# Kernel tuning notes

Measured on AMD Instinct MI355X. Metric: run time of the kernel, lower is better.

The kernel has to match this reference:

```python
import jax, jax.numpy as jnp
import numpy as np

HIDDEN = 896
N_HEADS = 14
N_KV = 2
HEAD_DIM = HIDDEN // N_HEADS  # 64
N_REP = N_HEADS // N_KV       # 7
ROPE_THETA = 1000000.0


def setup_inputs() -> dict:
    key = jax.random.key(0)
    ks = jax.random.split(key, 8)
    B, S = 2, 2048
    s = 0.02
    return {
        "hidden_states": jax.random.normal(ks[0], (B, S, HIDDEN), dtype=jnp.float32),
        "position_ids": jnp.broadcast_to(jnp.arange(S, dtype=jnp.int64), (B, S)),
        "Wq": jax.random.normal(ks[1], (HIDDEN, HIDDEN), dtype=jnp.float32) * s,
        "bq": jnp.zeros((HIDDEN,), dtype=jnp.float32),
        "Wk": jax.random.normal(ks[2], (N_KV * HEAD_DIM, HIDDEN), dtype=jnp.float32) * s,
        "bk": jnp.zeros((N_KV * HEAD_DIM,), dtype=jnp.float32),
        "Wv": jax.random.normal(ks[3], (N_KV * HEAD_DIM, HIDDEN), dtype=jnp.float32) * s,
        "bv": jnp.zeros((N_KV * HEAD_DIM,), dtype=jnp.float32),
        "Wo": jax.random.normal(ks[4], (HIDDEN, HIDDEN), dtype=jnp.float32) * s,
    }


def _rotate_half(x):
    x1, x2 = x[..., : HEAD_DIM // 2], x[..., HEAD_DIM // 2 :]
    return jnp.concatenate((-x2, x1), axis=-1)


def reference(hidden_states, position_ids, Wq, bq, Wk, bk, Wv, bv, Wo):
    B, S, _ = hidden_states.shape
    q = (hidden_states @ Wq.T + bq).reshape(B, S, N_HEADS, HEAD_DIM)
    k = (hidden_states @ Wk.T + bk).reshape(B, S, N_KV, HEAD_DIM)
    v = (hidden_states @ Wv.T + bv).reshape(B, S, N_KV, HEAD_DIM)

    # RoPE: cos/sin [B, S, 1, HEAD_DIM]
    inv_freq = 1.0 / (ROPE_THETA ** (jnp.arange(0, HEAD_DIM, 2, dtype=jnp.float32) / HEAD_DIM))
    freqs = position_ids.astype(jnp.float32)[..., None] * inv_freq  # [B,S,D/2]
    emb = jnp.concatenate((freqs, freqs), axis=-1)
    cos = jnp.cos(emb)[:, :, None, :]
    sin = jnp.sin(emb)[:, :, None, :]
    q = q * cos + _rotate_half(q) * sin
    k = k * cos + _rotate_half(k) * sin

    # [B, H, S, D]; repeat KV heads (GQA)
    q = q.transpose(0, 2, 1, 3)
    k = jnp.repeat(k.transpose(0, 2, 1, 3), N_REP, axis=1)
    v = jnp.repeat(v.transpose(0, 2, 1, 3), N_REP, axis=1)

    scale = 1.0 / np.sqrt(HEAD_DIM)
    scores = jnp.einsum("bhqd,bhkd->bhqk", q, k) * scale
    causal = jnp.tril(jnp.ones((S, S), dtype=bool))
    scores = jnp.where(causal[None, None, :, :], scores, jnp.finfo(scores.dtype).min)
    probs = jax.nn.softmax(scores, axis=-1)
    attn = jnp.einsum("bhqk,bhkd->bhqd", probs, v)  # [B,H,S,D]
    attn = attn.transpose(0, 2, 1, 3).reshape(B, S, HIDDEN)
    return attn @ Wo.T
```

## Files before the change

kernel.cpp:

```cpp
#include <hip/hip_runtime.h>

#define HID 896
#define NH 14
#define NKV 2
#define NREP 7
#define SEQ 2048
#define BT 2
#define NTOK (BT*SEQ)
#define CSCALE 0.18033688011112042f

typedef __attribute__((ext_vector_type(8))) short bf16x8;
typedef __attribute__((ext_vector_type(8))) unsigned short u16x8;
typedef __attribute__((ext_vector_type(4))) float fx4;
typedef __attribute__((ext_vector_type(4))) short s16x4;
typedef _Float16 f16x4 __attribute__((ext_vector_type(4)));
typedef __fp16 fp16x2 __attribute__((ext_vector_type(2)));

__device__ __forceinline__ unsigned short f2b(float x){
  union { float f; unsigned u; } a; a.f = x;
  unsigned r = a.u + 0x7FFFu + ((a.u >> 16) & 1u);
  return (unsigned short)(r >> 16);
}
__device__ __forceinline__ unsigned short f2h(float x){
  union { _Float16 h; unsigned short u; } a; a.h = (_Float16)x; return a.u;
}

__global__ __launch_bounds__(256) void cvt_kernel(
    const float* __restrict__ s0, const float* __restrict__ s1,
    const float* __restrict__ s2, const float* __restrict__ s3,
    const float* __restrict__ s4,
    unsigned short* __restrict__ d0, unsigned short* __restrict__ d1,
    unsigned short* __restrict__ d2, unsigned short* __restrict__ d3,
    unsigned short* __restrict__ d4,
    int c0, int c1, int c2, int c3, int c4)
{
  const float* s; unsigned short* d; int c;
  switch (blockIdx.y){
    case 0: s=s0; d=d0; c=c0; break;
    case 1: s=s1; d=d1; c=c1; break;
    case 2: s=s2; d=d2; c=c2; break;
    case 3: s=s3; d=d3; c=c3; break;
    default: s=s4; d=d4; c=c4; break;
  }
  for (int i = (blockIdx.x*256 + threadIdx.x)*8; i < c; i += gridDim.x*2048){
    float4 a = *(const float4*)(s + i);
    float4 b = *(const float4*)(s + i + 4);
    u16x8 o;
    o[0]=f2b(a.x); o[1]=f2b(a.y); o[2]=f2b(a.z); o[3]=f2b(a.w);
    o[4]=f2b(b.x); o[5]=f2b(b.y); o[6]=f2b(b.z); o[7]=f2b(b.w);
    *(u16x8*)(d + i) = o;
  }
}

__global__ __launch_bounds__(256) void qkv_gemm_kernel(
    const unsigned short* __restrict__ A, const unsigned short* __restrict__ Bw,
    const float* __restrict__ bq, const float* __restrict__ bk, const float* __restrict__ bv,
    const int* __restrict__ pos,
    unsigned short* __restrict__ qo, unsigned short* __restrict__ ko,
    unsigned short* __restrict__ vt)
{
  __shared__ short As[64*72];
  __shared__ short Bs[128*72];
  const int tid = threadIdx.x;
  const int bm = blockIdx.x, bn = blockIdx.y;
  const int w = tid >> 6, l = tid & 63, l15 = l & 15, q4 = l >> 4;
  const int wm = w >> 1, wn = w & 1;

  fx4 acc[2][4] = {};

  const int srow = tid >> 3, scol = (tid & 7)*8;
  const unsigned short* Ag = A  + (size_t)(bm*64  + srow)*HID + scol;
  const unsigned short* Bg = Bw + (size_t)(bn*128 + srow)*HID + scol;

  u16x8 ar[2], br[4];
#pragma unroll
  for (int p = 0; p < 2; p++) ar[p] = *(const u16x8*)(Ag + (size_t)p*32*HID);
#pragma unroll
  for (int p = 0; p < 4; p++) br[p] = *(const u16x8*)(Bg + (size_t)p*32*HID);

  for (int kt = 0; kt < 14; kt++){
#pragma unroll
    for (int p = 0; p < 2; p++) *(u16x8*)&As[(srow + p*32)*72 + scol] = ar[p];
#pragma unroll
    for (int p = 0; p < 4; p++) *(u16x8*)&Bs[(srow + p*32)*72 + scol] = br[p];
    __syncthreads();
    if (kt < 13){
      const int ko_ = (kt+1)*64;
#pragma unroll
      for (int p = 0; p < 2; p++) ar[p] = *(const u16x8*)(Ag + (size_t)p*32*HID + ko_);
#pragma unroll
      for (int p = 0; p < 4; p++) br[p] = *(const u16x8*)(Bg + (size_t)p*32*HID + ko_);
    }
#pragma unroll
    for (int ks = 0; ks < 2; ks++){
      bf16x8 af[2], bf[4];
#pragma unroll
      for (int mt = 0; mt < 2; mt++)
        af[mt] = *(bf16x8*)&As[(wm*32 + mt*16 + l15)*72 + ks*32 + q4*8];
#pragma unroll
      for (int nt = 0; nt < 4; nt++)
        bf[nt] = *(bf16x8*)&Bs[(wn*64 + nt*16 + l15)*72 + ks*32 + q4*8];
#pragma unroll
      for (int mt = 0; mt < 2; mt++)
#pragma unroll
        for (int nt = 0; nt < 4; nt++)
          acc[mt][nt] = __builtin_amdgcn_mfma_f32_16x16x32_bf16(af[mt], bf[nt], acc[mt][nt], 0,0,0);
    }
    __syncthreads();
  }

  const int hu = bn*2 + wn;
  const float* bias; int kind, hloc;
  if (hu < NH)      { bias = bq + hu*64;      kind = 0; hloc = hu; }
  else if (hu < 16) { bias = bk + (hu-NH)*64; kind = 1; hloc = hu-NH; }
  else              { bias = bv + (hu-16)*64; kind = 2; hloc = hu-16; }
  float bl[4];
#pragma unroll
  for (int nt = 0; nt < 4; nt++) bl[nt] = bias[nt*16 + l15];

  if (kind == 2){
#pragma unroll
    for (int mt = 0; mt < 2; mt++)
#pragma unroll
      for (int j = 0; j < 4; j++){
        int grow = bm*64 + wm*32 + mt*16 + q4*4 + j;
        int b = grow >> 11, s = grow & (SEQ-1);
        int tile = s >> 6, key = s & 63;
        unsigned short* dst = vt + (size_t)(((b*NKV + hloc)*(SEQ/64) + tile)*4096);
#pragma unroll
        for (int nt = 0; nt < 4; nt++)
          dst[(nt*16 + l15)*64 + key] = f2h(acc[mt][nt][j] + bl[nt]);
      }
  } else {
    float invf[2];
#pragma unroll
    for (int nt = 0; nt < 2; nt++)
      invf[nt] = exp2f(-(float)(nt*16 + l15) * 0.62286151779138041f);
#pragma unroll
    for (int mt = 0; mt < 2; mt++)
#pragma unroll
      for (int j = 0; j < 4; j++){
        int grow = bm*64 + wm*32 + mt*16 + q4*4 + j;
        int b = grow >> 11, s = grow & (SEQ-1);
        float p = (float)pos[grow];
        unsigned short* dst = (kind == 0)
            ? qo + ((size_t)(b*NH  + hloc)*SEQ + s)*64
            : ko + ((size_t)(b*NKV + hloc)*SEQ + s)*64;
#pragma unroll
        for (int nt = 0; nt < 2; nt++){
          int d = nt*16 + l15;
          float f = p * invf[nt];
          float sv, cv;
          sincosf(f, &sv, &cv);
          float x1 = acc[mt][nt][j]   + bl[nt];
          float x2 = acc[mt][nt+2][j] + bl[nt+2];
          dst[d]    = f2b(x1*cv - x2*sv);
          dst[d+32] = f2b(x2*cv + x1*sv);
        }
      }
  }
}

__device__ __forceinline__ void smax_pv(
    const fx4* s, bool diag, int wl, int q4,
    float& m_run, float& l_run, fx4* o, const f16x4 vf[4][4])
{
  float tv[16];
#pragma unroll
  for (int tl = 0; tl < 4; tl++)
#pragma unroll
    for (int j = 0; j < 4; j++){
      float x = s[tl][j]*CSCALE;
      if (diag && (tl*16 + q4*4 + j > wl)) x = -1e30f;
      tv[tl*4+j] = x;
    }
  float mx = tv[0];
#pragma unroll
  for (int i = 1; i < 16; i++) mx = fmaxf(mx, tv[i]);
  mx = fmaxf(mx, __shfl_xor(mx, 16));
  mx = fmaxf(mx, __shfl_xor(mx, 32));
  float mn = fmaxf(m_run, mx);
  float al = exp2f(m_run - mn);
  m_run = mn;
  float p[16], rs = 0.f;
#pragma unroll
  for (int i = 0; i < 16; i++){ p[i] = exp2f(tv[i] - mn); rs += p[i]; }
  rs += __shfl_xor(rs, 16);
  rs += __shfl_xor(rs, 32);
  l_run = l_run*al + rs;
#pragma unroll
  for (int nt = 0; nt < 4; nt++)
#pragma unroll
    for (int j = 0; j < 4; j++) o[nt][j] *= al;
  f16x4 pf[4];
#pragma unroll
  for (int tl = 0; tl < 4; tl++){
    union { f16x4 v; fp16x2 h[2]; } u;
    u.h[0] = __builtin_amdgcn_cvt_pkrtz(p[tl*4+0], p[tl*4+1]);
    u.h[1] = __builtin_amdgcn_cvt_pkrtz(p[tl*4+2], p[tl*4+3]);
    pf[tl] = u.v;
  }
#pragma unroll
  for (int nt = 0; nt < 4; nt++)
#pragma unroll
    for (int tl = 0; tl < 4; tl++)
      o[nt] = __builtin_amdgcn_mfma_f32_16x16x16f16(vf[nt][tl], pf[tl], o[nt], 0,0,0);
}

__global__ __launch_bounds__(512) void attn_kernel(
    const unsigned short* __restrict__ q, const unsigned short* __restrict__ k,
    const unsigned short* __restrict__ vt, unsigned short* __restrict__ ao)
{
  __shared__ short SB[4*64*72];
  short* KsB = SB;
  short* VtB = SB + 2*64*72;

  const int tid = threadIdx.x;
  const int w = tid >> 6, l = tid & 63, l15 = l & 15, q4 = l >> 4;
  const int g = w >> 2, wi = w & 3;
  const int tlo = blockIdx.x, thi = 31 - tlo;
  const int h = blockIdx.y, b = blockIdx.z, kvh = h / NREP;
  const int wl = wi*16 + l15;

  const unsigned short* qbase = q + ((size_t)(b*NH + h)*SEQ)*64;
  const unsigned short* qpA = qbase + (size_t)(thi*64 + wl)*64;
  const unsigned short* qpB = qbase + (size_t)(tlo*64 + wl)*64;
  bf16x8 qA0 = *(const bf16x8*)(qpA + q4*8), qA1 = *(const bf16x8*)(qpA + 32 + q4*8);
  bf16x8 qB0 = *(const bf16x8*)(qpB + q4*8), qB1 = *(const bf16x8*)(qpB + 32 + q4*8);

  fx4 oA[4] = {}, oB[4] = {};
  float mA = -1e30f, lA = 0.f, mB = -1e30f, lB = 0.f;

  const unsigned short* kbase = k  + ((size_t)(b*NKV + kvh)*SEQ)*64;
  const unsigned short* vbase = vt + (size_t)((b*NKV + kvh)*(SEQ/64))*4096;

  const int P = (thi + 2) >> 1;

  u16x8 kreg[2], vreg[2];
#pragma unroll
  for (int p = 0; p < 2; p++){
    int idx = p*512 + tid, tile = idx >> 9, off = idx & 511;
    kreg[p] = *(const u16x8*)(kbase + (size_t)tile*4096 + off*8);
    vreg[p] = *(const u16x8*)(vbase + (size_t)tile*4096 + off*8);
  }

  for (int si = 0; si < P; si++){
#pragma unroll
    for (int p = 0; p < 2; p++){
      int idx = p*512 + tid, tile = idx >> 9, off = idx & 511;
      int rr = off >> 3, g8 = off & 7;
      *(u16x8*)&KsB[tile*4608 + rr*72 + g8*8] = kreg[p];
      *(u16x8*)&VtB[tile*4608 + rr*72 + g8*8] = vreg[p];
    }
    __syncthreads();

    if (si + 1 < P){
      const int k0n = 2*(si+1);
#pragma unroll
      for (int p = 0; p < 2; p++){
        int idx = p*512 + tid, tile = idx >> 9, off = idx & 511;
        int tk = k0n + tile; if (tk > thi) tk = thi;
        kreg[p] = *(const u16x8*)(kbase + (size_t)tk*4096 + off*8);
        vreg[p] = *(const u16x8*)(vbase + (size_t)tk*4096 + off*8);
      }
    }

    const int kt = 2*si + g;
    if (kt <= thi){
      const short* Kst = KsB + g*4608;
      const short* Vtt = VtB + g*4608;
      bf16x8 kf0[4], kf1[4];
#pragma unroll
      for (int tl = 0; tl < 4; tl++){
        kf0[tl] = *(const bf16x8*)&Kst[(tl*16 + l15)*72 + q4*8];
        kf1[tl] = *(const bf16x8*)&Kst[(tl*16 + l15)*72 + 32 + q4*8];
      }
      f16x4 vf[4][4];
#pragma unroll
      for (int nt = 0; nt < 4; nt++)
#pragma unroll
        for (int tl = 0; tl < 4; tl++)
          vf[nt][tl] = *(const f16x4*)&Vtt[(nt*16 + l15)*72 + tl*16 + q4*4];

      {
        fx4 s[4] = {};
#pragma unroll
        for (int tl = 0; tl < 4; tl++){
          s[tl] = __builtin_amdgcn_mfma_f32_16x16x32_bf16(kf0[tl], qA0, s[tl], 0,0,0);
          s[tl] = __builtin_amdgcn_mfma_f32_16x16x32_bf16(kf1[tl], qA1, s[tl], 0,0,0);
        }
        smax_pv(s, kt == thi, wl, q4, mA, lA, oA, vf);
      }
      if (kt <= tlo){
        fx4 s[4] = {};
#pragma unroll
        for (int tl = 0; tl < 4; tl++){
          s[tl] = __builtin_amdgcn_mfma_f32_16x16x32_bf16(kf0[tl], qB0, s[tl], 0,0,0);
          s[tl] = __builtin_amdgcn_mfma_f32_16x16x32_bf16(kf1[tl], qB1, s[tl], 0,0,0);
        }
        smax_pv(s, kt == tlo, wl, q4, mB, lB, oB, vf);
      }
    }
    __syncthreads();
  }

  float* F = (float*)SB;
  if (g == 1){
    float* fa = F + (((wi*2 + 0)*64 + l)*18);
#pragma unroll
    for (int nt = 0; nt < 4; nt++)
#pragma unroll
      for (int j = 0; j < 4; j++) fa[nt*4 + j] = oA[nt][j];
    fa[16] = mA; fa[17] = lA;
    float* fb = F + (((wi*2 + 1)*64 + l)*18);
#pragma unroll
    for (int nt = 0; nt < 4; nt++)
#pragma unroll
      for (int j = 0; j < 4; j++) fb[nt*4 + j] = oB[nt][j];
    fb[16] = mB; fb[17] = lB;
  }
  __syncthreads();
  if (g == 0){
    {
      const float* fa = F + (((wi*2 + 0)*64 + l)*18);
      float m1 = fa[16], l1 = fa[17];
      float mM = fmaxf(mA, m1);
      float a0 = exp2f(mA - mM), a1 = exp2f(m1 - mM);
      lA = lA*a0 + l1*a1;
#pragma unroll
      for (int nt = 0; nt < 4; nt++)
#pragma unroll
        for (int j = 0; j < 4; j++) oA[nt][j] = oA[nt][j]*a0 + fa[nt*4+j]*a1;
    }
    {
      const float* fb = F + (((wi*2 + 1)*64 + l)*18);
      float m1 = fb[16], l1 = fb[17];
      float mM = fmaxf(mB, m1);
      float a0 = exp2f(mB - mM), a1 = exp2f(m1 - mM);
      lB = lB*a0 + l1*a1;
#pragma unroll
      for (int nt = 0; nt < 4; nt++)
#pragma unroll
        for (int j = 0; j < 4; j++) oB[nt][j] = oB[nt][j]*a0 + fb[nt*4+j]*a1;
    }
    {
      float inv = 1.0f / lA;
      unsigned short* dst = ao + ((size_t)(b*SEQ + thi*64 + wl))*HID + h*64;
#pragma unroll
      for (int nt = 0; nt < 4; nt++){
        s16x4 ov;
        ov[0] = (short)f2b(oA[nt][0]*inv); ov[1] = (short)f2b(oA[nt][1]*inv);
        ov[2] = (short)f2b(oA[nt][2]*inv); ov[3] = (short)f2b(oA[nt][3]*inv);
        *(s16x4*)(dst + nt*16 + q4*4) = ov;
      }
    }
    {
      float inv = 1.0f / lB;
      unsigned short* dst = ao + ((size_t)(b*SEQ + tlo*64 + wl))*HID + h*64;
#pragma unroll
      for (int nt = 0; nt < 4; nt++){
        s16x4 ov;
        ov[0] = (short)f2b(oB[nt][0]*inv); ov[1] = (short)f2b(oB[nt][1]*inv);
        ov[2] = (short)f2b(oB[nt][2]*inv); ov[3] = (short)f2b(oB[nt][3]*inv);
        *(s16x4*)(dst + nt*16 + q4*4) = ov;
      }
    }
  }
}

__global__ __launch_bounds__(256) void out_gemm_kernel(
    const unsigned short* __restrict__ A, const unsigned short* __restrict__ Bw,
    float* __restrict__ out)
{
  __shared__ short As[64*72];
  __shared__ short Bs[128*72];
  const int tid = threadIdx.x;
  const int bm = blockIdx.x, bn = blockIdx.y;
  const int w = tid >> 6, l = tid & 63, l15 = l & 15, q4 = l >> 4;
  const int wm = w >> 1, wn = w & 1;

  fx4 acc[2][4] = {};

  const int srow = tid >> 3, scol = (tid & 7)*8;
  const unsigned short* Ag = A  + (size_t)(bm*64  + srow)*HID + scol;
  const unsigned short* Bg = Bw + (size_t)(bn*128 + srow)*HID + scol;

  u16x8 ar[2], br[4];
#pragma unroll
  for (int p = 0; p < 2; p++) ar[p] = *(const u16x8*)(Ag + (size_t)p*32*HID);
#pragma unroll
  for (int p = 0; p < 4; p++) br[p] = *(const u16x8*)(Bg + (size_t)p*32*HID);

  for (int kt = 0; kt < 14; kt++){
#pragma unroll
    for (int p = 0; p < 2; p++) *(u16x8*)&As[(srow + p*32)*72 + scol] = ar[p];
#pragma unroll
    for (int p = 0; p < 4; p++) *(u16x8*)&Bs[(srow + p*32)*72 + scol] = br[p];
    __syncthreads();
    if (kt < 13){
      const int ko_ = (kt+1)*64;
#pragma unroll
      for (int p = 0; p < 2; p++) ar[p] = *(const u16x8*)(Ag + (size_t)p*32*HID + ko_);
#pragma unroll
      for (int p = 0; p < 4; p++) br[p] = *(const u16x8*)(Bg + (size_t)p*32*HID + ko_);
    }
#pragma unroll
    for (int ks = 0; ks < 2; ks++){
      bf16x8 af[2], bf[4];
#pragma unroll
      for (int mt = 0; mt < 2; mt++)
        af[mt] = *(bf16x8*)&As[(wm*32 + mt*16 + l15)*72 + ks*32 + q4*8];
#pragma unroll
      for (int nt = 0; nt < 4; nt++)
        bf[nt] = *(bf16x8*)&Bs[(wn*64 + nt*16 + l15)*72 + ks*32 + q4*8];
#pragma unroll
      for (int mt = 0; mt < 2; mt++)
#pragma unroll
        for (int nt = 0; nt < 4; nt++)
          acc[mt][nt] = __builtin_amdgcn_mfma_f32_16x16x32_bf16(af[mt], bf[nt], acc[mt][nt], 0,0,0);
    }
    __syncthreads();
  }

#pragma unroll
  for (int mt = 0; mt < 2; mt++)
#pragma unroll
    for (int j = 0; j < 4; j++){
      int grow = bm*64 + wm*32 + mt*16 + q4*4 + j;
      float* dst = out + (size_t)grow*HID + bn*128 + wn*64;
#pragma unroll
      for (int nt = 0; nt < 4; nt++)
        dst[nt*16 + l15] = acc[mt][nt][j];
    }
}

extern "C" void kernel_launch(void* const* d_in, const int* in_sizes, int n_in,
                              void* d_out, int out_size, void* d_ws, size_t ws_size,
                              hipStream_t stream)
{
  const float* hidden = (const float*)d_in[0];
  const int*   pos    = (const int*)d_in[1];
  const float* Wq = (const float*)d_in[2]; const float* bq = (const float*)d_in[3];
  const float* Wk = (const float*)d_in[4]; const float* bk = (const float*)d_in[5];
  const float* Wv = (const float*)d_in[6]; const float* bv = (const float*)d_in[7];
  const float* Wo = (const float*)d_in[8];

  unsigned short* qws   = (unsigned short*)d_ws;
  unsigned short* kws   = qws   + (size_t)BT*NH*SEQ*64;
  unsigned short* vtws  = kws   + (size_t)BT*NKV*SEQ*64;
  unsigned short* wqkv  = vtws  + (size_t)BT*NKV*SEQ*64;
  unsigned short* wo16  = wqkv  + (size_t)1152*HID;
  unsigned short* h16   = wo16  + (size_t)HID*HID;

  const int nh   = NTOK*HID;
  const int nwq  = HID*HID;
  const int nwkv = 2*64*HID;

  cvt_kernel<<<dim3(448, 5), 256, 0, stream>>>(
      hidden, Wq, Wk, Wv, Wo,
      h16, wqkv, wqkv + nwq, wqkv + nwq + nwkv, wo16,
      nh, nwq, nwkv, nwkv, nwq);

  qkv_gemm_kernel<<<dim3(NTOK/64, 9), 256, 0, stream>>>(
      h16, wqkv, bq, bk, bv, pos, qws, kws, vtws);

  attn_kernel<<<dim3(16, NH, BT), 512, 0, stream>>>(qws, kws, vtws, h16 );

  out_gemm_kernel<<<dim3(NTOK/64, 7), 256, 0, stream>>>(h16 , wo16, (float*)d_out);
}
```

Baseline: 171.7 us.

## Fuse hidden-state bf16 conversion into QKV GEMM, precompute RoPE table, fold scale

Removes the separate fp32-to-bf16 conversion pass over hidden states by loading fp32 directly in the QKV GEMM and converting while staging into shared memory. A cos/sin RoPE table is built in the weight-conversion kernel so the GEMM epilogue does lookups instead of sincosf. The softmax scale is folded into Q in the epilogue, and both GEMMs move to a 128-wide K tile with 7 iterations instead of 14. The cost is more registers for the larger staging buffers, larger LDS tiles, and a table indexed by position that assumes positions are below SEQ.

```diff
diff --git a/kernel.cpp b/kernel.cpp
--- a/kernel.cpp
+++ b/kernel.cpp
@@ -16,6 +16,8 @@
 typedef _Float16 f16x4 __attribute__((ext_vector_type(4)));
 typedef __fp16 fp16x2 __attribute__((ext_vector_type(2)));
 
+#define LDA 136
+
 __device__ __forceinline__ unsigned short f2b(float x){
   union { float f; unsigned u; } a; a.f = x;
   unsigned r = a.u + 0x7FFFu + ((a.u >> 16) & 1u);
@@ -28,19 +30,26 @@
 __global__ __launch_bounds__(256) void cvt_kernel(
     const float* __restrict__ s0, const float* __restrict__ s1,
     const float* __restrict__ s2, const float* __restrict__ s3,
-    const float* __restrict__ s4,
     unsigned short* __restrict__ d0, unsigned short* __restrict__ d1,
     unsigned short* __restrict__ d2, unsigned short* __restrict__ d3,
-    unsigned short* __restrict__ d4,
-    int c0, int c1, int c2, int c3, int c4)
-{
+    int c0, int c1, int c2, int c3,
+    float2* __restrict__ tab)
+{
+  if (blockIdx.y == 4){
+    for (int i = blockIdx.x*256 + threadIdx.x; i < SEQ*32; i += gridDim.x*256){
+      int s = i >> 5, d = i & 31;
+      float f = (float)s * exp2f(-(float)d * 0.62286151779138041f);
+      float sv, cv; sincosf(f, &sv, &cv);
+      tab[i] = make_float2(cv, sv);
+    }
+    return;
+  }
   const float* s; unsigned short* d; int c;
   switch (blockIdx.y){
     case 0: s=s0; d=d0; c=c0; break;
     case 1: s=s1; d=d1; c=c1; break;
     case 2: s=s2; d=d2; c=c2; break;
-    case 3: s=s3; d=d3; c=c3; break;
-    default: s=s4; d=d4; c=c4; break;
+    default: s=s3; d=d3; c=c3; break;
   }
   for (int i = (blockIdx.x*256 + threadIdx.x)*8; i < c; i += gridDim.x*2048){
     float4 a = *(const float4*)(s + i);
@@ -53,14 +62,14 @@
 }
 
 __global__ __launch_bounds__(256) void qkv_gemm_kernel(
-    const unsigned short* __restrict__ A, const unsigned short* __restrict__ Bw,
+    const float* __restrict__ hidden, const unsigned short* __restrict__ Bw,
     const float* __restrict__ bq, const float* __restrict__ bk, const float* __restrict__ bv,
-    const int* __restrict__ pos,
+    const int* __restrict__ pos, const float2* __restrict__ tab,
     unsigned short* __restrict__ qo, unsigned short* __restrict__ ko,
     unsigned short* __restrict__ vt)
 {
-  __shared__ short As[64*72];
-  __shared__ short Bs[128*72];
+  __shared__ short As[64*LDA];
+  __shared__ short Bs[128*LDA];
   const int tid = threadIdx.x;
   const int bm = blockIdx.x, bn = blockIdx.y;
   const int w = tid >> 6, l = tid & 63, l15 = l & 15, q4 = l >> 4;
@@ -68,38 +77,44 @@
 
   fx4 acc[2][4] = {};
 
-  const int srow = tid >> 3, scol = (tid & 7)*8;
-  const unsigned short* Ag = A  + (size_t)(bm*64  + srow)*HID + scol;
-  const unsigned short* Bg = Bw + (size_t)(bn*128 + srow)*HID + scol;
-
-  u16x8 ar[2], br[4];
-#pragma unroll
-  for (int p = 0; p < 2; p++) ar[p] = *(const u16x8*)(Ag + (size_t)p*32*HID);
-#pragma unroll
-  for (int p = 0; p < 4; p++) br[p] = *(const u16x8*)(Bg + (size_t)p*32*HID);
-
-  for (int kt = 0; kt < 14; kt++){
-#pragma unroll
-    for (int p = 0; p < 2; p++) *(u16x8*)&As[(srow + p*32)*72 + scol] = ar[p];
-#pragma unroll
-    for (int p = 0; p < 4; p++) *(u16x8*)&Bs[(srow + p*32)*72 + scol] = br[p];
-    __syncthreads();
-    if (kt < 13){
-      const int ko_ = (kt+1)*64;
-#pragma unroll
-      for (int p = 0; p < 2; p++) ar[p] = *(const u16x8*)(Ag + (size_t)p*32*HID + ko_);
-#pragma unroll
-      for (int p = 0; p < 4; p++) br[p] = *(const u16x8*)(Bg + (size_t)p*32*HID + ko_);
-    }
-#pragma unroll
-    for (int ks = 0; ks < 2; ks++){
+  const int arow = tid >> 2, acol = (tid & 3)*32;
+  const int brow = tid >> 1, bcol = (tid & 1)*64;
+  const float* Agf = hidden + (size_t)(bm*64 + arow)*HID + acol;
+  const unsigned short* Bg = Bw + (size_t)(bn*128 + brow)*HID + bcol;
+
+  float4 a4[8]; u16x8 br[8];
+#pragma unroll
+  for (int p = 0; p < 8; p++) a4[p] = *(const float4*)(Agf + p*4);
+#pragma unroll
+  for (int p = 0; p < 8; p++) br[p] = *(const u16x8*)(Bg + p*8);
+
+  for (int kt = 0; kt < 7; kt++){
+#pragma unroll
+    for (int p = 0; p < 4; p++){
+      u16x8 av;
+      av[0]=f2b(a4[2*p].x); av[1]=f2b(a4[2*p].y); av[2]=f2b(a4[2*p].z); av[3]=f2b(a4[2*p].w);
+      av[4]=f2b(a4[2*p+1].x); av[5]=f2b(a4[2*p+1].y); av[6]=f2b(a4[2*p+1].z); av[7]=f2b(a4[2*p+1].w);
+      *(u16x8*)&As[arow*LDA + acol + p*8] = av;
+    }
+#pragma unroll
+    for (int p = 0; p < 8; p++) *(u16x8*)&Bs[brow*LDA + bcol + p*8] = br[p];
+    __syncthreads();
+    if (kt < 6){
+      const int ko_ = (kt+1)*128;
+#pragma unroll
+      for (int p = 0; p < 8; p++) a4[p] = *(const float4*)(Agf + ko_ + p*4);
+#pragma unroll
+      for (int p = 0; p < 8; p++) br[p] = *(const u16x8*)(Bg + ko_ + p*8);
+    }
+#pragma unroll
+    for (int ks = 0; ks < 4; ks++){
       bf16x8 af[2], bf[4];
 #pragma unroll
       for (int mt = 0; mt < 2; mt++)
-        af[mt] = *(bf16x8*)&As[(wm*32 + mt*16 + l15)*72 + ks*32 + q4*8];
-#pragma unroll
-      for (int nt = 0; nt < 4; nt++)
-        bf[nt] = *(bf16x8*)&Bs[(wn*64 + nt*16 + l15)*72 + ks*32 + q4*8];
+        af[mt] = *(bf16x8*)&As[(wm*32 + mt*16 + l15)*LDA + ks*32 + q4*8];
+#pragma unroll
+      for (int nt = 0; nt < 4; nt++)
+        bf[nt] = *(bf16x8*)&Bs[(wn*64 + nt*16 + l15)*LDA + ks*32 + q4*8];
 #pragma unroll
       for (int mt = 0; mt < 2; mt++)
 #pragma unroll
@@ -132,31 +147,25 @@
           dst[(nt*16 + l15)*64 + key] = f2h(acc[mt][nt][j] + bl[nt]);
       }
   } else {
-    float invf[2];
-#pragma unroll
-    for (int nt = 0; nt < 2; nt++)
-      invf[nt] = exp2f(-(float)(nt*16 + l15) * 0.62286151779138041f);
+    const float qs = (kind == 0) ? CSCALE : 1.0f;
 #pragma unroll
     for (int mt = 0; mt < 2; mt++)
 #pragma unroll
       for (int j = 0; j < 4; j++){
         int grow = bm*64 + wm*32 + mt*16 + q4*4 + j;
         int b = grow >> 11, s = grow & (SEQ-1);
-        float p = (float)pos[grow];
+        int p = pos[grow];
+        const float2* rp = tab + p*32 + l15;
+        float2 cs0 = rp[0], cs1 = rp[16];
         unsigned short* dst = (kind == 0)
             ? qo + ((size_t)(b*NH  + hloc)*SEQ + s)*64
             : ko + ((size_t)(b*NKV + hloc)*SEQ + s)*64;
-#pragma unroll
-        for (int nt = 0; nt < 2; nt++){
-          int d = nt*16 + l15;
-          float f = p * invf[nt];
-          float sv, cv;
-          sincosf(f, &sv, &cv);
-          float x1 = acc[mt][nt][j]   + bl[nt];
-          float x2 = acc[mt][nt+2][j] + bl[nt+2];
-          dst[d]    = f2b(x1*cv - x2*sv);
-          dst[d+32] = f2b(x2*cv + x1*sv);
-        }
+        float x1 = acc[mt][0][j] + bl[0], x2 = acc[mt][2][j] + bl[2];
+        float y1 = acc[mt][1][j] + bl[1], y2 = acc[mt][3][j] + bl[3];
+        dst[l15]      = f2b((x1*cs0.x - x2*cs0.y)*qs);
+        dst[16 + l15] = f2b((y1*cs1.x - y2*cs1.y)*qs);
+        dst[32 + l15] = f2b((x2*cs0.x + x1*cs0.y)*qs);
+        dst[48 + l15] = f2b((y2*cs1.x + y1*cs1.y)*qs);
       }
   }
 }
@@ -170,7 +179,7 @@
   for (int tl = 0; tl < 4; tl++)
 #pragma unroll
     for (int j = 0; j < 4; j++){
-      float x = s[tl][j]*CSCALE;
+      float x = s[tl][j];
       if (diag && (tl*16 + q4*4 + j > wl)) x = -1e30f;
       tv[tl*4+j] = x;
     }
@@ -372,8 +381,8 @@
     const unsigned short* __restrict__ A, const unsigned short* __restrict__ Bw,
     float* __restrict__ out)
 {
-  __shared__ short As[64*72];
-  __shared__ short Bs[128*72];
+  __shared__ short As[64*LDA];
+  __shared__ short Bs[128*LDA];
   const int tid = threadIdx.x;
   const int bm = blockIdx.x, bn = blockIdx.y;
   const int w = tid >> 6, l = tid & 63, l15 = l & 15, q4 = l >> 4;
@@ -381,38 +390,39 @@
 
   fx4 acc[2][4] = {};
 
-  const int srow = tid >> 3, scol = (tid & 7)*8;
-  const unsigned short* Ag = A  + (size_t)(bm*64  + srow)*HID + scol;
-  const unsigned short* Bg = Bw + (size_t)(bn*128 + srow)*HID + scol;
-
-  u16x8 ar[2], br[4];
-#pragma unroll
-  for (int p = 0; p < 2; p++) ar[p] = *(const u16x8*)(Ag + (size_t)p*32*HID);
-#pragma unroll
-  for (int p = 0; p < 4; p++) br[p] = *(const u16x8*)(Bg + (size_t)p*32*HID);
-
-  for (int kt = 0; kt < 14; kt++){
-#pragma unroll
-    for (int p = 0; p < 2; p++) *(u16x8*)&As[(srow + p*32)*72 + scol] = ar[p];
-#pragma unroll
-    for (int p = 0; p < 4; p++) *(u16x8*)&Bs[(srow + p*32)*72 + scol] = br[p];
-    __syncthreads();
-    if (kt < 13){
-      const int ko_ = (kt+1)*64;
-#pragma unroll
-      for (int p = 0; p < 2; p++) ar[p] = *(const u16x8*)(Ag + (size_t)p*32*HID + ko_);
-#pragma unroll
-      for (int p = 0; p < 4; p++) br[p] = *(const u16x8*)(Bg + (size_t)p*32*HID + ko_);
-    }
-#pragma unroll
-    for (int ks = 0; ks < 2; ks++){
+  const int arow = tid >> 2, acol = (tid & 3)*32;
+  const int brow = tid >> 1, bcol = (tid & 1)*64;
+  const unsigned short* Ag = A  + (size_t)(bm*64  + arow)*HID + acol;
+  const unsigned short* Bg = Bw + (size_t)(bn*128 + brow)*HID + bcol;
+
+  u16x8 ar[4], br[8];
+#pragma unroll
+  for (int p = 0; p < 4; p++) ar[p] = *(const u16x8*)(Ag + p*8);
+#pragma unroll
+  for (int p = 0; p < 8; p++) br[p] = *(const u16x8*)(Bg + p*8);
+
+  for (int kt = 0; kt < 7; kt++){
+#pragma unroll
+    for (int p = 0; p < 4; p++) *(u16x8*)&As[arow*LDA + acol + p*8] = ar[p];
+#pragma unroll
+    for (int p = 0; p < 8; p++) *(u16x8*)&Bs[brow*LDA + bcol + p*8] = br[p];
+    __syncthreads();
+    if (kt < 6){
+      const int ko_ = (kt+1)*128;
+#pragma unroll
+      for (int p = 0; p < 4; p++) ar[p] = *(const u16x8*)(Ag + ko_ + p*8);
+#pragma unroll
+      for (int p = 0; p < 8; p++) br[p] = *(const u16x8*)(Bg + ko_ + p*8);
+    }
+#pragma unroll
+    for (int ks = 0; ks < 4; ks++){
       bf16x8 af[2], bf[4];
 #pragma unroll
       for (int mt = 0; mt < 2; mt++)
-        af[mt] = *(bf16x8*)&As[(wm*32 + mt*16 + l15)*72 + ks*32 + q4*8];
-#pragma unroll
-      for (int nt = 0; nt < 4; nt++)
-        bf[nt] = *(bf16x8*)&Bs[(wn*64 + nt*16 + l15)*72 + ks*32 + q4*8];
+        af[mt] = *(bf16x8*)&As[(wm*32 + mt*16 + l15)*LDA + ks*32 + q4*8];
+#pragma unroll
+      for (int nt = 0; nt < 4; nt++)
+        bf[nt] = *(bf16x8*)&Bs[(wn*64 + nt*16 + l15)*LDA + ks*32 + q4*8];
 #pragma unroll
       for (int mt = 0; mt < 2; mt++)
 #pragma unroll
@@ -451,20 +461,20 @@
   unsigned short* wqkv  = vtws  + (size_t)BT*NKV*SEQ*64;
   unsigned short* wo16  = wqkv  + (size_t)1152*HID;
   unsigned short* h16   = wo16  + (size_t)HID*HID;
-
-  const int nh   = NTOK*HID;
+  float2*         tab   = (float2*)(h16 + (size_t)NTOK*HID);
+
   const int nwq  = HID*HID;
   const int nwkv = 2*64*HID;
 
-  cvt_kernel<<<dim3(448, 5), 256, 0, stream>>>(
-      hidden, Wq, Wk, Wv, Wo,
-      h16, wqkv, wqkv + nwq, wqkv + nwq + nwkv, wo16,
-      nh, nwq, nwkv, nwkv, nwq);
+  cvt_kernel<<<dim3(392, 5), 256, 0, stream>>>(
+      Wq, Wk, Wv, Wo,
+      wqkv, wqkv + nwq, wqkv + nwq + nwkv, wo16,
+      nwq, nwkv, nwkv, nwq, tab);
 
   qkv_gemm_kernel<<<dim3(NTOK/64, 9), 256, 0, stream>>>(
-      h16, wqkv, bq, bk, bv, pos, qws, kws, vtws);
-
-  attn_kernel<<<dim3(16, NH, BT), 512, 0, stream>>>(qws, kws, vtws, h16 );
-
-  out_gemm_kernel<<<dim3(NTOK/64, 7), 256, 0, stream>>>(h16 , wo16, (float*)d_out);
-}
+      hidden, wqkv, bq, bk, bv, pos, tab, qws, kws, vtws);
+
+  attn_kernel<<<dim3(16, NH, BT), 512, 0, stream>>>(qws, kws, vtws, h16);
+
+  out_gemm_kernel<<<dim3(NTOK/64, 7), 256, 0, stream>>>(h16, wo16, (float*)d_out);
+}
```

Result: slower. 201.4 us (+17.3%).

## Fuse fp32-to-bf16 conversion into GEMM loads and fold softmax scale into Q

Applied to the files above, without the earlier changes.

Removes the separate conversion kernel and instead loads fp32 hidden states and weights directly in the QKV and output GEMMs, converting to bf16 before the shared-memory store. The softmax scale constant is folded into the Q RoPE epilogue, so the attention kernel no longer multiplies every score. This saves a kernel launch and a full write/read of bf16 copies, but doubles the global bytes each GEMM tile loads and repeats the weight conversion across many blocks. The RoPE epilogue is also restructured to write all four 16-column groups per row.

```diff
diff --git a/kernel.cpp b/kernel.cpp
--- a/kernel.cpp
+++ b/kernel.cpp
@@ -24,36 +24,16 @@
 __device__ __forceinline__ unsigned short f2h(float x){
   union { _Float16 h; unsigned short u; } a; a.h = (_Float16)x; return a.u;
 }
-
-__global__ __launch_bounds__(256) void cvt_kernel(
-    const float* __restrict__ s0, const float* __restrict__ s1,
-    const float* __restrict__ s2, const float* __restrict__ s3,
-    const float* __restrict__ s4,
-    unsigned short* __restrict__ d0, unsigned short* __restrict__ d1,
-    unsigned short* __restrict__ d2, unsigned short* __restrict__ d3,
-    unsigned short* __restrict__ d4,
-    int c0, int c1, int c2, int c3, int c4)
-{
-  const float* s; unsigned short* d; int c;
-  switch (blockIdx.y){
-    case 0: s=s0; d=d0; c=c0; break;
-    case 1: s=s1; d=d1; c=c1; break;
-    case 2: s=s2; d=d2; c=c2; break;
-    case 3: s=s3; d=d3; c=c3; break;
-    default: s=s4; d=d4; c=c4; break;
-  }
-  for (int i = (blockIdx.x*256 + threadIdx.x)*8; i < c; i += gridDim.x*2048){
-    float4 a = *(const float4*)(s + i);
-    float4 b = *(const float4*)(s + i + 4);
-    u16x8 o;
-    o[0]=f2b(a.x); o[1]=f2b(a.y); o[2]=f2b(a.z); o[3]=f2b(a.w);
-    o[4]=f2b(b.x); o[5]=f2b(b.y); o[6]=f2b(b.z); o[7]=f2b(b.w);
-    *(u16x8*)(d + i) = o;
-  }
+__device__ __forceinline__ u16x8 cvt8(float4 a, float4 b){
+  u16x8 o;
+  o[0]=f2b(a.x); o[1]=f2b(a.y); o[2]=f2b(a.z); o[3]=f2b(a.w);
+  o[4]=f2b(b.x); o[5]=f2b(b.y); o[6]=f2b(b.z); o[7]=f2b(b.w);
+  return o;
 }
 
 __global__ __launch_bounds__(256) void qkv_gemm_kernel(
-    const unsigned short* __restrict__ A, const unsigned short* __restrict__ Bw,
+    const float* __restrict__ hidden,
+    const float* __restrict__ Wq, const float* __restrict__ Wk, const float* __restrict__ Wv,
     const float* __restrict__ bq, const float* __restrict__ bk, const float* __restrict__ bv,
     const int* __restrict__ pos,
     unsigned short* __restrict__ qo, unsigned short* __restrict__ ko,
@@ -68,28 +48,44 @@
 
   fx4 acc[2][4] = {};
 
+  const float* Wsrc = (bn < 7) ? Wq + (size_t)(bn*128)*HID : ((bn == 7) ? Wk : Wv);
+
   const int srow = tid >> 3, scol = (tid & 7)*8;
-  const unsigned short* Ag = A  + (size_t)(bm*64  + srow)*HID + scol;
-  const unsigned short* Bg = Bw + (size_t)(bn*128 + srow)*HID + scol;
-
-  u16x8 ar[2], br[4];
-#pragma unroll
-  for (int p = 0; p < 2; p++) ar[p] = *(const u16x8*)(Ag + (size_t)p*32*HID);
-#pragma unroll
-  for (int p = 0; p < 4; p++) br[p] = *(const u16x8*)(Bg + (size_t)p*32*HID);
+  const float* Agf = hidden + (size_t)(bm*64 + srow)*HID + scol;
+  const float* Bgf = Wsrc + (size_t)srow*HID + scol;
+
+  float4 a0[2], a1[2], b0[4], b1[4];
+#pragma unroll
+  for (int p = 0; p < 2; p++){
+    a0[p] = *(const float4*)(Agf + (size_t)p*32*HID);
+    a1[p] = *(const float4*)(Agf + (size_t)p*32*HID + 4);
+  }
+#pragma unroll
+  for (int p = 0; p < 4; p++){
+    b0[p] = *(const float4*)(Bgf + (size_t)p*32*HID);
+    b1[p] = *(const float4*)(Bgf + (size_t)p*32*HID + 4);
+  }
 
   for (int kt = 0; kt < 14; kt++){
 #pragma unroll
-    for (int p = 0; p < 2; p++) *(u16x8*)&As[(srow + p*32)*72 + scol] = ar[p];
-#pragma unroll
-    for (int p = 0; p < 4; p++) *(u16x8*)&Bs[(srow + p*32)*72 + scol] = br[p];
+    for (int p = 0; p < 2; p++)
+      *(u16x8*)&As[(srow + p*32)*72 + scol] = cvt8(a0[p], a1[p]);
+#pragma unroll
+    for (int p = 0; p < 4; p++)
+      *(u16x8*)&Bs[(srow + p*32)*72 + scol] = cvt8(b0[p], b1[p]);
     __syncthreads();
     if (kt < 13){
       const int ko_ = (kt+1)*64;
 #pragma unroll
-      for (int p = 0; p < 2; p++) ar[p] = *(const u16x8*)(Ag + (size_t)p*32*HID + ko_);
-#pragma unroll
-      for (int p = 0; p < 4; p++) br[p] = *(const u16x8*)(Bg + (size_t)p*32*HID + ko_);
+      for (int p = 0; p < 2; p++){
+        a0[p] = *(const float4*)(Agf + (size_t)p*32*HID + ko_);
+        a1[p] = *(const float4*)(Agf + (size_t)p*32*HID + ko_ + 4);
+      }
+#pragma unroll
+      for (int p = 0; p < 4; p++){
+        b0[p] = *(const float4*)(Bgf + (size_t)p*32*HID + ko_);
+        b1[p] = *(const float4*)(Bgf + (size_t)p*32*HID + ko_ + 4);
+      }
     }
 #pragma unroll
     for (int ks = 0; ks < 2; ks++){
@@ -132,6 +128,7 @@
           dst[(nt*16 + l15)*64 + key] = f2h(acc[mt][nt][j] + bl[nt]);
       }
   } else {
+    const float qs = (kind == 0) ? CSCALE : 1.0f;
     float invf[2];
 #pragma unroll
     for (int nt = 0; nt < 2; nt++)
@@ -146,17 +143,15 @@
         unsigned short* dst = (kind == 0)
             ? qo + ((size_t)(b*NH  + hloc)*SEQ + s)*64
             : ko + ((size_t)(b*NKV + hloc)*SEQ + s)*64;
-#pragma unroll
-        for (int nt = 0; nt < 2; nt++){
-          int d = nt*16 + l15;
-          float f = p * invf[nt];
-          float sv, cv;
-          sincosf(f, &sv, &cv);
-          float x1 = acc[mt][nt][j]   + bl[nt];
-          float x2 = acc[mt][nt+2][j] + bl[nt+2];
-          dst[d]    = f2b(x1*cv - x2*sv);
-          dst[d+32] = f2b(x2*cv + x1*sv);
-        }
+        float x1 = acc[mt][0][j] + bl[0], x2 = acc[mt][2][j] + bl[2];
+        float y1 = acc[mt][1][j] + bl[1], y2 = acc[mt][3][j] + bl[3];
+        float s0v, c0v, s1v, c1v;
+        sincosf(p*invf[0], &s0v, &c0v);
+        sincosf(p*invf[1], &s1v, &c1v);
+        dst[l15]      = f2b((x1*c0v - x2*s0v)*qs);
+        dst[16 + l15] = f2b((y1*c1v - y2*s1v)*qs);
+        dst[32 + l15] = f2b((x2*c0v + x1*s0v)*qs);
+        dst[48 + l15] = f2b((y2*c1v + y1*s1v)*qs);
       }
   }
 }
@@ -170,7 +165,7 @@
   for (int tl = 0; tl < 4; tl++)
 #pragma unroll
     for (int j = 0; j < 4; j++){
-      float x = s[tl][j]*CSCALE;
+      float x = s[tl][j];
       if (diag && (tl*16 + q4*4 + j > wl)) x = -1e30f;
       tv[tl*4+j] = x;
     }
@@ -369,7 +364,7 @@
 }
 
 __global__ __launch_bounds__(256) void out_gemm_kernel(
-    const unsigned short* __restrict__ A, const unsigned short* __restrict__ Bw,
+    const unsigned short* __restrict__ A, const float* __restrict__ Wo,
     float* __restrict__ out)
 {
   __shared__ short As[64*72];
@@ -382,27 +377,33 @@
   fx4 acc[2][4] = {};
 
   const int srow = tid >> 3, scol = (tid & 7)*8;
-  const unsigned short* Ag = A  + (size_t)(bm*64  + srow)*HID + scol;
-  const unsigned short* Bg = Bw + (size_t)(bn*128 + srow)*HID + scol;
-
-  u16x8 ar[2], br[4];
+  const unsigned short* Ag = A + (size_t)(bm*64 + srow)*HID + scol;
+  const float* Bgf = Wo + (size_t)(bn*128 + srow)*HID + scol;
+
+  u16x8 ar[2]; float4 b0[4], b1[4];
 #pragma unroll
   for (int p = 0; p < 2; p++) ar[p] = *(const u16x8*)(Ag + (size_t)p*32*HID);
 #pragma unroll
-  for (int p = 0; p < 4; p++) br[p] = *(const u16x8*)(Bg + (size_t)p*32*HID);
+  for (int p = 0; p < 4; p++){
+    b0[p] = *(const float4*)(Bgf + (size_t)p*32*HID);
+    b1[p] = *(const float4*)(Bgf + (size_t)p*32*HID + 4);
+  }
 
   for (int kt = 0; kt < 14; kt++){
 #pragma unroll
     for (int p = 0; p < 2; p++) *(u16x8*)&As[(srow + p*32)*72 + scol] = ar[p];
 #pragma unroll
-    for (int p = 0; p < 4; p++) *(u16x8*)&Bs[(srow + p*32)*72 + scol] = br[p];
+    for (int p = 0; p < 4; p++) *(u16x8*)&Bs[(srow + p*32)*72 + scol] = cvt8(b0[p], b1[p]);
     __syncthreads();
     if (kt < 13){
       const int ko_ = (kt+1)*64;
 #pragma unroll
       for (int p = 0; p < 2; p++) ar[p] = *(const u16x8*)(Ag + (size_t)p*32*HID + ko_);
 #pragma unroll
-      for (int p = 0; p < 4; p++) br[p] = *(const u16x8*)(Bg + (size_t)p*32*HID + ko_);
+      for (int p = 0; p < 4; p++){
+        b0[p] = *(const float4*)(Bgf + (size_t)p*32*HID + ko_);
+        b1[p] = *(const float4*)(Bgf + (size_t)p*32*HID + ko_ + 4);
+      }
     }
 #pragma unroll
     for (int ks = 0; ks < 2; ks++){
@@ -445,26 +446,15 @@
   const float* Wv = (const float*)d_in[6]; const float* bv = (const float*)d_in[7];
   const float* Wo = (const float*)d_in[8];
 
-  unsigned short* qws   = (unsigned short*)d_ws;
-  unsigned short* kws   = qws   + (size_t)BT*NH*SEQ*64;
-  unsigned short* vtws  = kws   + (size_t)BT*NKV*SEQ*64;
-  unsigned short* wqkv  = vtws  + (size_t)BT*NKV*SEQ*64;
-  unsigned short* wo16  = wqkv  + (size_t)1152*HID;
-  unsigned short* h16   = wo16  + (size_t)HID*HID;
-
-  const int nh   = NTOK*HID;
-  const int nwq  = HID*HID;
-  const int nwkv = 2*64*HID;
-
-  cvt_kernel<<<dim3(448, 5), 256, 0, stream>>>(
-      hidden, Wq, Wk, Wv, Wo,
-      h16, wqkv, wqkv + nwq, wqkv + nwq + nwkv, wo16,
-      nh, nwq, nwkv, nwkv, nwq);
+  unsigned short* qws  = (unsigned short*)d_ws;
+  unsigned short* kws  = qws  + (size_t)BT*NH*SEQ*64;
+  unsigned short* vtws = kws  + (size_t)BT*NKV*SEQ*64;
+  unsigned short* aws  = vtws + (size_t)BT*NKV*SEQ*64;
 
   qkv_gemm_kernel<<<dim3(NTOK/64, 9), 256, 0, stream>>>(
-      h16, wqkv, bq, bk, bv, pos, qws, kws, vtws);
-
-  attn_kernel<<<dim3(16, NH, BT), 512, 0, stream>>>(qws, kws, vtws, h16 );
-
-  out_gemm_kernel<<<dim3(NTOK/64, 7), 256, 0, stream>>>(h16 , wo16, (float*)d_out);
-}
+      hidden, Wq, Wk, Wv, bq, bk, bv, pos, qws, kws, vtws);
+
+  attn_kernel<<<dim3(16, NH, BT), 512, 0, stream>>>(qws, kws, vtws, aws);
+
+  out_gemm_kernel<<<dim3(NTOK/64, 7), 256, 0, stream>>>(aws, Wo, (float*)d_out);
+}
```

After: 175.2 us. About the same (+2.0%).
